# Kernel tuning notes

Measured on AMD Instinct MI355X. Metric: run time of the kernel, lower is better.

The kernel has to match this reference:

```python
import jax, jax.numpy as jnp
import numpy as np

B, S, NC, ND, V = 16, 512, 10000, 10000, 128


def _rn(k, shape, scale=0.05):
    return jax.random.normal(k, shape, dtype=jnp.float32) * scale


def setup_inputs() -> dict:
    key = jax.random.key(0)
    ks = jax.random.split(key, 24)
    inp = {
        'c_seq': jax.random.randint(ks[0], (B, S), 0, NC),
        'd_seq': jax.random.randint(ks[1], (B, S), 0, ND),
        'r_seq': jax.random.uniform(ks[2], (B, S), dtype=jnp.float32),
        # embeddings / vectors
        'D1_w': _rn(ks[3], (ND, 1)),
        'D2_w': _rn(ks[4], (ND, V)),
        'v_r': _rn(ks[5], (V,)),
        'v_beta': _rn(ks[6], (V,)),
        # GRU (torch layout: gates ordered r,z,n; W_ih [3V,2V], W_hh [3V,V])
        'W_ih': _rn(ks[7], (3 * V, 2 * V)),
        'W_hh': _rn(ks[8], (3 * V, V)),
        'b_ih': jnp.zeros((3 * V,), jnp.float32),
        'b_hh': jnp.zeros((3 * V,), jnp.float32),
        # linear_1: V -> V -> V -> 1 (weights stored [in, out])
        'm1_W1': _rn(ks[9], (V, V)), 'm1_b1': jnp.zeros((V,), jnp.float32),
        'm1_W2': _rn(ks[10], (V, V)), 'm1_b2': jnp.zeros((V,), jnp.float32),
        'm1_W3': _rn(ks[11], (V, 1)), 'm1_b3': jnp.zeros((1,), jnp.float32),
        # linear_2: 3V -> V -> V -> 1
        'm2_W1': _rn(ks[12], (3 * V, V)), 'm2_b1': jnp.zeros((V,), jnp.float32),
        'm2_W2': _rn(ks[13], (V, V)), 'm2_b2': jnp.zeros((V,), jnp.float32),
        'm2_W3': _rn(ks[14], (V, 1)), 'm2_b3': jnp.zeros((1,), jnp.float32),
    }
    return inp


def _mlp(x, W1, b1, W2, b2, W3, b3):
    h = jax.nn.relu(x @ W1 + b1)
    h = jax.nn.relu(h @ W2 + b2)
    return h @ W3 + b3


def _gru_seq(x, W_ih, W_hh, b_ih, b_hh):
    # x: [B,S,2V] -> h_seq [B,S,V]; torch GRU gate order r,z,n
    xp = x @ W_ih.T + b_ih  # [B,S,3V]

    def step(h, xt):
        hp = h @ W_hh.T + b_hh
        xr, xz, xn = jnp.split(xt, 3, axis=-1)
        hr, hz, hn = jnp.split(hp, 3, axis=-1)
        r = jax.nn.sigmoid(xr + hr)
        z = jax.nn.sigmoid(xz + hz)
        n = jnp.tanh(xn + r * hn)
        h_new = (1.0 - z) * n + z * h
        return h_new, h_new

    h0 = jnp.zeros((x.shape[0], W_hh.shape[1]), x.dtype)
    _, hs = jax.lax.scan(step, h0, jnp.swapaxes(xp, 0, 1))  # [S,B,V]
    return jnp.swapaxes(hs, 0, 1)


def reference(c_seq, d_seq, r_seq, D1_w, D2_w, v_r, v_beta,
              W_ih, W_hh, b_ih, b_hh,
              m1_W1, m1_b1, m1_W2, m1_b2, m1_W3, m1_b3,
              m2_W1, m2_b1, m2_W2, m2_b2, m2_W3, m2_b3):
    v_d_seq = D2_w[d_seq]                     # [B,S,V]
    v_r_seq = r_seq[..., None] * v_r          # [B,S,V]

    h_seq = _gru_seq(jnp.concatenate([v_d_seq, v_r_seq], axis=-1),
                     W_ih, W_hh, b_ih, b_hh)  # [B,S,V]
    alpha_seq = _mlp(h_seq, m1_W1, m1_b1, m1_W2, m1_b2, m1_W3, m1_b3)[..., 0]  # [B,S]

    bidx = jnp.arange(c_seq.shape[0])

    def step(C, ins):
        c_t, vd_t, vr_t = ins                 # [B], [B,V], [B,V]
        beta_prev = C[bidx, c_t]              # gather: [B]
        v_beta_prev = beta_prev[:, None] * v_beta  # [B,V]
        new_c = _mlp(jnp.concatenate([v_beta_prev, vd_t, vr_t], axis=-1),
                     m2_W1, m2_b1, m2_W2, m2_b2, m2_W3, m2_b3)[:, 0]  # [B]
        C = C.at[bidx, c_t].set(new_c)        # scatter
        return C, (C, new_c)

    C0 = jnp.zeros((c_seq.shape[0], NC), jnp.float32)
    _, (C_seq, beta_seq) = jax.lax.scan(
        step, C0,
        (jnp.swapaxes(c_seq, 0, 1), jnp.swapaxes(v_d_seq, 0, 1), jnp.swapaxes(v_r_seq, 0, 1)))
    C_seq = jnp.swapaxes(C_seq, 0, 1)[..., None]   # [B,S,NC,1]
    beta_seq = jnp.swapaxes(beta_seq, 0, 1)        # [B,S]

    gamma_seq = D1_w[d_seq][..., 0]                # [B,S]
    return (alpha_seq, beta_seq, gamma_seq, h_seq, C_seq)
```

## Files before the change

### kernel.cpp

```cpp
#include <hip/hip_runtime.h>

#define Bq   16
#define Sq   512
#define Vq   128
#define NCq  10000

typedef __attribute__((ext_vector_type(8))) short short8v;
typedef __attribute__((ext_vector_type(4))) float f32x4;

#define OFF_P1B_U  3145728u
#define OFF_WTIH   2097152u
#define OFF_WVRIH  2146304u
#define OFF_WVR1   2146688u
#define OFF_WVB    2146816u
#define OFF_PO     2146944u

#define PLN 136
#define PLSZ (16*PLN+8)

__device__ __forceinline__ unsigned short f2bf(float x) {
    unsigned u = __builtin_bit_cast(unsigned, x);
    unsigned r = (u + 0x7fffu + ((u >> 16) & 1u)) >> 16;
    return (unsigned short)r;
}
__device__ __forceinline__ float bfhi(unsigned u) {
    return __builtin_bit_cast(float, u << 16);
}
__device__ __forceinline__ float bflo(unsigned u) {
    return __builtin_bit_cast(float, u & 0xffff0000u);
}
__device__ __forceinline__ void gload_lds16(const void* g, void* l) {
    __builtin_amdgcn_global_load_lds(
        (const __attribute__((address_space(1))) unsigned int*)g,
        (__attribute__((address_space(3))) unsigned int*)l, 16, 0, 0);
}

__global__ __launch_bounds__(256) void k0_prep(
    const int* __restrict__ c_seq, const int* __restrict__ d_seq,
    const float* __restrict__ D1_w,
    const float* __restrict__ W_ih,
    const float* __restrict__ v_r, const float* __restrict__ v_beta,
    const float* __restrict__ m2W1,
    float* __restrict__ ws, float* __restrict__ gamma_out)
{
    const int blk = blockIdx.x, tid = threadIdx.x;

    if (blk < 128) {
        float* WTIH = ws + OFF_WTIH;
        int base = blk * 384;
        for (int i = tid; i < 384; i += 256) {
            int e = base + i;
            int k = e / 384, g = e % 384;
            WTIH[e] = W_ih[g * 256 + k];
        }
    } else if (blk == 128) {
        float* WVRIH = ws + OFF_WVRIH;
        float* WVR1  = ws + OFF_WVR1;
        float* WVB   = ws + OFF_WVB;
        for (int g = tid; g < 384; g += 256) {
            float a = 0.f;
            for (int k = 0; k < 128; ++k) a = fmaf(v_r[k], W_ih[g * 256 + 128 + k], a);
            WVRIH[g] = a;
        }
        if (tid < 128) {
            float a = 0.f, b = 0.f;
            for (int k = 0; k < 128; ++k) {
                a = fmaf(v_r[k],    m2W1[(256 + k) * 128 + tid], a);
                b = fmaf(v_beta[k], m2W1[k * 128 + tid],         b);
            }
            WVR1[tid] = a; WVB[tid] = b;
        }
    } else if (blk < 145) {
        const int b = blk - 129;
        __shared__ int cs[Sq];
        for (int i = tid; i < Sq; i += 256) cs[i] = c_seq[b * Sq + i];
        __syncthreads();
        int* PO = (int*)(ws + OFF_PO);
        for (int t = tid; t < Sq; t += 256) {
            int c = cs[t];
            int po = -1;
            for (int u = t - 1; u >= 0; --u) if (cs[u] == c) { po = u; break; }
            PO[t * 16 + b] = po;
        }
    } else {
        const int b = blk - 145;
        for (int s = tid; s < Sq; s += 256)
            gamma_out[b * Sq + s] = D1_w[d_seq[b * Sq + s]];
    }
}

__global__ __launch_bounds__(256) void k1_gemm(
    const int* __restrict__ d_seq, const float* __restrict__ D2_w,
    const float* __restrict__ m2W1,
    const float* __restrict__ b_ih, const float* __restrict__ b_hh,
    const float* __restrict__ r_seq, const float* __restrict__ m2b1,
    float* __restrict__ ws)
{
    __shared__ float As[64 * 128];
    __shared__ float Bs[128 * 64];
    const int blk = blockIdx.x, tid = threadIdx.x;
    const int nc = blk & 7;
    const int m0 = (blk >> 3) * 64;
    const float* WTIH = ws + OFF_WTIH;

    const float4* D2v = (const float4*)D2_w;
    for (int e = tid; e < 2048; e += 256) {
        int r = e >> 5, q = e & 31;
        int d = d_seq[m0 + r];
        *(float4*)&As[r * 128 + 4 * q] = D2v[d * 32 + q];
    }
    for (int e = tid; e < 2048; e += 256) {
        int k = e >> 4, q = e & 15;
        float4 v;
        if (nc < 6) v = *(const float4*)&WTIH[k * 384 + nc * 64 + 4 * q];
        else        v = *(const float4*)&m2W1[(128 + k) * 128 + (nc - 6) * 64 + 4 * q];
        *(float4*)&Bs[k * 64 + 4 * q] = v;
    }
    __syncthreads();

    const int tx = tid & 15, ty = tid >> 4;
    const int c0 = 4 * tx, r0 = 4 * ty;
    float acc[4][4];
#pragma unroll
    for (int i = 0; i < 4; ++i)
#pragma unroll
        for (int j = 0; j < 4; ++j) acc[i][j] = 0.f;

    for (int k = 0; k < 128; ++k) {
        float4 bv = *(const float4*)&Bs[k * 64 + c0];
#pragma unroll
        for (int i = 0; i < 4; ++i) {
            float a = As[(r0 + i) * 128 + k];
            acc[i][0] = fmaf(a, bv.x, acc[i][0]);
            acc[i][1] = fmaf(a, bv.y, acc[i][1]);
            acc[i][2] = fmaf(a, bv.z, acc[i][2]);
            acc[i][3] = fmaf(a, bv.w, acc[i][3]);
        }
    }

    float rsv[4];
#pragma unroll
    for (int i = 0; i < 4; ++i) rsv[i] = r_seq[m0 + r0 + i];

    if (nc < 6) {
        const int grow0 = nc * 64 + c0;
        float4 bi  = *(const float4*)&b_ih[grow0];
        float4 wv4 = *(const float4*)&(ws + OFF_WVRIH)[grow0];
        float4 bh4 = make_float4(0.f, 0.f, 0.f, 0.f);
        if (nc < 4) bh4 = *(const float4*)&b_hh[grow0];
        unsigned short* XPB = (unsigned short*)ws;
        const int r4 = grow0 >> 2;
#pragma unroll
        for (int i = 0; i < 4; ++i) {
            int row = m0 + r0 + i;
            int t = row & 511, bb = row >> 9;
            float vx = acc[i][0] + bi.x + bh4.x + rsv[i] * wv4.x;
            float vy = acc[i][1] + bi.y + bh4.y + rsv[i] * wv4.y;
            float vz = acc[i][2] + bi.z + bh4.z + rsv[i] * wv4.z;
            float vw = acc[i][3] + bi.w + bh4.w + rsv[i] * wv4.w;
            uint2 p;
            p.x = (unsigned)f2bf(vx) | ((unsigned)f2bf(vy) << 16);
            p.y = (unsigned)f2bf(vz) | ((unsigned)f2bf(vw) << 16);
            *(uint2*)&XPB[((size_t)((bb >> 2) * 512 + t)) * 1536 + r4 * 16 + (bb & 3) * 4] = p;
        }
    } else {
        const int j0 = (nc - 6) * 64 + c0;
        float4 b1v = *(const float4*)&m2b1[j0];
        float4 wr1 = *(const float4*)&(ws + OFF_WVR1)[j0];
        unsigned short* P1B = (unsigned short*)ws + OFF_P1B_U;
#pragma unroll
        for (int i = 0; i < 4; ++i) {
            int row = m0 + r0 + i;
            int t = row & 511, bb = row >> 9;
            float vx = acc[i][0] + b1v.x + rsv[i] * wr1.x;
            float vy = acc[i][1] + b1v.y + rsv[i] * wr1.y;
            float vz = acc[i][2] + b1v.z + rsv[i] * wr1.z;
            float vw = acc[i][3] + b1v.w + rsv[i] * wr1.w;
            uint2 p;
            p.x = (unsigned)f2bf(vx) | ((unsigned)f2bf(vy) << 16);
            p.y = (unsigned)f2bf(vz) | ((unsigned)f2bf(vw) << 16);
            *(uint2*)&P1B[((size_t)(t * 16 + bb)) * 128 + j0] = p;
        }
    }
}

__global__ __launch_bounds__(512, 1) void k2_scan(
    const float* __restrict__ W_hh, const float* __restrict__ b_hh,
    const float* __restrict__ m2W2, const float* __restrict__ m2b2,
    const float* __restrict__ m2W3, const float* __restrict__ m2b3,
    float* __restrict__ ws,
    float* __restrict__ hseq_out, float* __restrict__ beta_out)
{
    __shared__ __align__(16) unsigned char smem[23040];
    const int tid = threadIdx.x;
    const int l = tid & 63, wv = tid >> 6;
    const int qq = l >> 4, cb = l & 15;
    const int bgid = blockIdx.x;

    if (bgid < 4) {
        unsigned short* hP  = (unsigned short*)smem;
        unsigned short* xps = (unsigned short*)(smem + 4 * PLSZ);
        const unsigned short* XPB = (const unsigned short*)ws;

        short8v aH[3][4];
#pragma unroll
        for (int g = 0; g < 3; ++g) {
            const float* wrow = W_hh + (g * 128 + 16 * wv + cb) * 128;
#pragma unroll
            for (int kf = 0; kf < 4; ++kf) {
                short8v hi;
#pragma unroll
                for (int e = 0; e < 8; ++e) hi[e] = (short)f2bf(wrow[kf * 32 + qq * 8 + e]);
                aH[g][kf] = hi;
            }
        }
        float bhn[4];
        *(float4*)bhn = *(const float4*)&b_hh[256 + 16 * wv + 4 * qq];
        float hold[4] = {0.f, 0.f, 0.f, 0.f};

        for (int i = tid; i < 2 * PLSZ; i += 512) hP[i] = 0;
        if (wv < 3) {
            const unsigned short* src = XPB + ((size_t)(bgid * 512)) * 1536 + wv * 512 + l * 8;
            gload_lds16(src, xps + wv * 512);
        }
        __syncthreads();

        for (int t = 0; t < 512; ++t) {
            if (t < 511 && wv < 3) {
                const unsigned short* src =
                    XPB + ((size_t)(bgid * 512 + t + 1)) * 1536 + wv * 512 + l * 8;
                gload_lds16(src, xps + ((t + 1) & 1) * 1536 + wv * 512);
            }
            const unsigned short* xcur = xps + (t & 1) * 1536;
            f32x4 px[3];
#pragma unroll
            for (int g = 0; g < 3; ++g) {
                uint2 u = *(const uint2*)(xcur + (32 * g + 4 * wv + qq) * 16 + (cb & 3) * 4);
                px[g][0] = bfhi(u.x); px[g][1] = bflo(u.x);
                px[g][2] = bfhi(u.y); px[g][3] = bflo(u.y);
            }
            const unsigned short* HI = hP + (t & 1) * PLSZ;
            unsigned short* HIn = hP + ((t + 1) & 1) * PLSZ;

            f32x4 C0 = {0.f,0.f,0.f,0.f}, C1 = {0.f,0.f,0.f,0.f}, C2 = {0.f,0.f,0.f,0.f};
#pragma unroll
            for (int kf = 0; kf < 4; ++kf) {
                short8v Bh = *(const short8v*)(HI + cb * PLN + kf * 32 + qq * 8);
                C0 = __builtin_amdgcn_mfma_f32_16x16x32_bf16(aH[0][kf], Bh, C0, 0, 0, 0);
                C1 = __builtin_amdgcn_mfma_f32_16x16x32_bf16(aH[1][kf], Bh, C1, 0, 0, 0);
                C2 = __builtin_amdgcn_mfma_f32_16x16x32_bf16(aH[2][kf], Bh, C2, 0, 0, 0);
            }
            float hnew[4];
#pragma unroll
            for (int i = 0; i < 4; ++i) {
                float pr = C0[i] + px[0][i];
                float pz = C1[i] + px[1][i];
                float r = 1.f / (1.f + __expf(-pr));
                float z = 1.f / (1.f + __expf(-pz));
                float hn = C2[i] + bhn[i];
                float npre = fmaf(r, hn, px[2][i]);
                float ax = fabsf(npre);
                float e2 = __expf(-2.f * ax);
                float n = copysignf((1.f - e2) / (1.f + e2), npre);
                float hv = (1.f - z) * n + z * hold[i];
                hold[i] = hv;
                hnew[i] = hv;
            }
            if (cb < 4) {
                *(float4*)&hseq_out[((size_t)((bgid * 4 + cb) * 512 + t)) * 128 + 16 * wv + 4 * qq] =
                    make_float4(hnew[0], hnew[1], hnew[2], hnew[3]);
                unsigned short h0 = f2bf(hnew[0]), h1 = f2bf(hnew[1]);
                unsigned short h2 = f2bf(hnew[2]), h3 = f2bf(hnew[3]);
                uint2 hw;
                hw.x = (unsigned)h0 | ((unsigned)h1 << 16);
                hw.y = (unsigned)h2 | ((unsigned)h3 << 16);
                *(uint2*)(HIn + cb * PLN + 16 * wv + 4 * qq) = hw;
            }
            __syncthreads();
        }
    } else {
        const int bq = bgid - 4;
        float* bhL = (float*)smem;
        int*   poT = (int*)(smem + 8192);
        unsigned short* h1P  = (unsigned short*)(smem + 16384);
        unsigned short* xpre = (unsigned short*)(smem + 20752);
        float* redL = (float*)(smem + 22800);
        const unsigned short* P1B = (const unsigned short*)ws + OFF_P1B_U;

        {
            const int* POg = (const int*)(ws + OFF_PO);
            for (int i = tid; i < 2048; i += 512)
                poT[i] = POg[(i >> 2) * 16 + 4 * bq + (i & 3)];
        }
        for (int i = tid; i < PLSZ; i += 512) h1P[i] = 0;
        if (wv == 0)
            gload_lds16(P1B + ((size_t)(4 * bq)) * 128 + l * 8, xpre);

        short8v aH[4];
#pragma unroll
        for (int kf = 0; kf < 4; ++kf) {
            short8v hi;
#pragma unroll
            for (int e = 0; e < 8; ++e)
                hi[e] = (short)f2bf(m2W2[(kf * 32 + qq * 8 + e) * 128 + 16 * wv + cb]);
            aH[kf] = hi;
        }
        float w3C[4], b2C[4];
        *(float4*)w3C = *(const float4*)&m2W3[16 * wv + 4 * qq];
        *(float4*)b2C = *(const float4*)&m2b2[16 * wv + 4 * qq];
        const float b3v = m2b3[0];

        const int bb2 = tid & 3, j4 = (tid >> 2) & 31;
        const bool pa = tid < 128;
        float wvb[4] = {0.f, 0.f, 0.f, 0.f};
        if (pa) *(float4*)wvb = *(const float4*)&(ws + OFF_WVB)[j4 * 4];
        float btap = 0.f;
        __syncthreads();

        for (int t = 0; t < 512; ++t) {
            if (pa) {
                int po = poT[t * 4 + bb2];
                float bp = (po == t - 1) ? btap : ((po >= 0) ? bhL[bb2 * 512 + po] : 0.f);
                uint2 u = *(const uint2*)(xpre + (t & 1) * 512 + bb2 * 128 + j4 * 4);
                float h0 = fmaxf(0.f, fmaf(bp, wvb[0], bfhi(u.x)));
                float h1 = fmaxf(0.f, fmaf(bp, wvb[1], bflo(u.x)));
                float h2 = fmaxf(0.f, fmaf(bp, wvb[2], bfhi(u.y)));
                float h3 = fmaxf(0.f, fmaf(bp, wvb[3], bflo(u.y)));
                uint2 hw;
                hw.x = (unsigned)f2bf(h0) | ((unsigned)f2bf(h1) << 16);
                hw.y = (unsigned)f2bf(h2) | ((unsigned)f2bf(h3) << 16);
                *(uint2*)(h1P + bb2 * PLN + j4 * 4) = hw;
            }
            if (tid < 4 && t > 0) bhL[tid * 512 + (t - 1)] = btap;
            __syncthreads();

            if (t < 511 && wv == 0)
                gload_lds16(P1B + ((size_t)((t + 1) * 16 + 4 * bq)) * 128 + l * 8,
                            xpre + ((t + 1) & 1) * 512);

            f32x4 C = {0.f, 0.f, 0.f, 0.f};
#pragma unroll
            for (int kf = 0; kf < 4; ++kf) {
                short8v Bh = *(const short8v*)(h1P + cb * PLN + kf * 32 + qq * 8);
                C = __builtin_amdgcn_mfma_f32_16x16x32_bf16(aH[kf], Bh, C, 0, 0, 0);
            }
            float part = 0.f;
#pragma unroll
            for (int i = 0; i < 4; ++i)
                part = fmaf(fmaxf(0.f, C[i] + b2C[i]), w3C[i], part);
            part += __shfl_xor(part, 16);
            part += __shfl_xor(part, 32);
            if (qq == 0 && cb < 4) redL[wv * 4 + cb] = part;
            __syncthreads();

            float bta = b3v;
#pragma unroll
            for (int w = 0; w < 8; ++w) bta += redL[w * 4 + (tid & 3)];
            btap = bta;
        }
        if (tid < 4) bhL[tid * 512 + 511] = btap;
        __syncthreads();
        for (int i = tid; i < 2048; i += 512)
            beta_out[(4 * bq + (i >> 9)) * 512 + (i & 511)] = bhL[i];
    }
}

__global__ __launch_bounds__(256) void k2b_fill(
    const int* __restrict__ c_seq, const float* __restrict__ beta_in,
    float* __restrict__ C_out)
{
    __shared__ int   scs[Sq];
    __shared__ float sbt[Sq];
    const int bid = blockIdx.x, tid = threadIdx.x;
    const int b = bid / 40, rem = bid % 40;
    const int chunk = rem >> 2, q = rem & 3;

    for (int i = tid; i < Sq; i += 256) {
        scs[i] = c_seq[b * Sq + i];
        sbt[i] = beta_in[b * Sq + i];
    }
    __syncthreads();

    const int c0 = chunk * 1024 + tid * 4;
    if (c0 >= NCq) return;

    float cur0 = 0.f, cur1 = 0.f, cur2 = 0.f, cur3 = 0.f;
    const int tlo = q * 128, thi = tlo + 128;
    float* base = C_out + (size_t)b * Sq * NCq + c0;

    for (int t = 0; t < tlo; ++t) {
        int ct = scs[t] - c0; float bv = sbt[t];
        cur0 = (ct == 0) ? bv : cur0;
        cur1 = (ct == 1) ? bv : cur1;
        cur2 = (ct == 2) ? bv : cur2;
        cur3 = (ct == 3) ? bv : cur3;
    }
    for (int t = tlo; t < thi; ++t) {
        int ct = scs[t] - c0; float bv = sbt[t];
        cur0 = (ct == 0) ? bv : cur0;
        cur1 = (ct == 1) ? bv : cur1;
        cur2 = (ct == 2) ? bv : cur2;
        cur3 = (ct == 3) ? bv : cur3;
        *(float4*)(base + (size_t)t * NCq) = make_float4(cur0, cur1, cur2, cur3);
    }
}

__global__ __launch_bounds__(256) void k3_alpha(
    const float* __restrict__ hseq,
    const float* __restrict__ W1, const float* __restrict__ b1,
    const float* __restrict__ W2, const float* __restrict__ b2,
    const float* __restrict__ W3, const float* __restrict__ b3,
    float* __restrict__ alpha_out)
{
    __shared__ float Hs[32 * 128];
    __shared__ float T1[32 * 128];
    __shared__ float red[4][16];
    const int blk = blockIdx.x, tid = threadIdx.x;
    const int row0 = blk * 32;

    for (int e = tid; e < 1024; e += 256) {
        int r = e >> 5, q = e & 31;
        *(float4*)&Hs[r * 128 + 4 * q] =
            *(const float4*)&hseq[(size_t)(row0 + r) * 128 + 4 * q];
    }
    __syncthreads();

    const int j = tid & 127, rh = tid >> 7;
    const float b1j = b1[j], b2j = b2[j], w3j = W3[j];
    float acc[16];
#pragma unroll
    for (int r = 0; r < 16; ++r) acc[r] = b1j;
    for (int k = 0; k < 128; ++k) {
        float w = W1[k * 128 + j];
#pragma unroll
        for (int r = 0; r < 16; ++r)
            acc[r] = fmaf(Hs[(rh * 16 + r) * 128 + k], w, acc[r]);
    }
#pragma unroll
    for (int r = 0; r < 16; ++r) {
        acc[r] = fmaxf(acc[r], 0.f);
        T1[(rh * 16 + r) * 128 + j] = acc[r];
    }
    __syncthreads();
    float acc2[16];
#pragma unroll
    for (int r = 0; r < 16; ++r) acc2[r] = b2j;
    for (int k = 0; k < 128; ++k) {
        float w = W2[k * 128 + j];
#pragma unroll
        for (int r = 0; r < 16; ++r)
            acc2[r] = fmaf(T1[(rh * 16 + r) * 128 + k], w, acc2[r]);
    }
#pragma unroll
    for (int r = 0; r < 16; ++r) {
        float p = fmaxf(acc2[r], 0.f) * w3j;
#pragma unroll
        for (int off = 1; off < 64; off <<= 1) p += __shfl_xor(p, off);
        if ((tid & 63) == 0) red[tid >> 6][r] = p;
    }
    __syncthreads();
    if (tid < 32) {
        int rr = tid & 15, g = tid >> 4;
        alpha_out[row0 + g * 16 + rr] = red[2 * g][rr] + red[2 * g + 1][rr] + b3[0];
    }
}

extern "C" void kernel_launch(void* const* d_in, const int* in_sizes, int n_in,
                              void* d_out, int out_size, void* d_ws, size_t ws_size,
                              hipStream_t stream) {
    const int*   c_seq = (const int*)d_in[0];
    const int*   d_seq = (const int*)d_in[1];
    const float* r_seq = (const float*)d_in[2];
    const float* D1_w  = (const float*)d_in[3];
    const float* D2_w  = (const float*)d_in[4];
    const float* v_r   = (const float*)d_in[5];
    const float* v_b   = (const float*)d_in[6];
    const float* W_ih  = (const float*)d_in[7];
    const float* W_hh  = (const float*)d_in[8];
    const float* b_ih  = (const float*)d_in[9];
    const float* b_hh  = (const float*)d_in[10];
    const float* m1W1  = (const float*)d_in[11];
    const float* m1b1  = (const float*)d_in[12];
    const float* m1W2  = (const float*)d_in[13];
    const float* m1b2  = (const float*)d_in[14];
    const float* m1W3  = (const float*)d_in[15];
    const float* m1b3  = (const float*)d_in[16];
    const float* m2W1  = (const float*)d_in[17];
    const float* m2b1  = (const float*)d_in[18];
    const float* m2W2  = (const float*)d_in[19];
    const float* m2b2  = (const float*)d_in[20];
    const float* m2W3  = (const float*)d_in[21];
    const float* m2b3  = (const float*)d_in[22];

    float* out   = (float*)d_out;
    float* alpha = out;
    float* beta  = out + 8192;
    float* gamma = out + 16384;
    float* hseq  = out + 24576;
    float* Cseq  = out + 1073152;
    float* ws    = (float*)d_ws;

    hipLaunchKernelGGL(k0_prep, dim3(161), dim3(256), 0, stream,
                       c_seq, d_seq, D1_w, W_ih, v_r, v_b, m2W1, ws, gamma);
    hipLaunchKernelGGL(k1_gemm, dim3(1024), dim3(256), 0, stream,
                       d_seq, D2_w, m2W1, b_ih, b_hh, r_seq, m2b1, ws);
    hipLaunchKernelGGL(k2_scan, dim3(8), dim3(512), 0, stream,
                       W_hh, b_hh, m2W2, m2b2, m2W3, m2b3, ws, hseq, beta);
    hipLaunchKernelGGL(k2b_fill, dim3(640), dim3(256), 0, stream,
                       c_seq, beta, Cseq);
    hipLaunchKernelGGL(k3_alpha, dim3(256), dim3(256), 0, stream,
                       hseq, m1W1, m1b1, m1W2, m1b2, m1W3, m1b3, alpha);
}
```

Measured before the change: 750.7 us.

## Register-prefetch scan inputs and use lightweight LDS-only barriers in recurrent scans

Both recurrent scan loops stop staging per-step inputs through LDS via global_load_lds and instead prefetch them two steps ahead into registers. __syncthreads is replaced by a barrier that only waits on LDS counters, so global loads and stores in flight no longer stall each step. The beta scan also drops the poT LDS table, loading previous-occurrence indices directly with lookahead, and uses a transposed reduction buffer read with float4. The gate math switches to hardware reciprocal approximations, which slightly changes precision. The lgkm-only barrier depends on the outstanding global loads being register-destined, not LDS-destined.

```diff
diff --git a/kernel.cpp b/kernel.cpp
--- a/kernel.cpp
+++ b/kernel.cpp
@@ -29,10 +29,11 @@
 __device__ __forceinline__ float bflo(unsigned u) {
     return __builtin_bit_cast(float, u & 0xffff0000u);
 }
-__device__ __forceinline__ void gload_lds16(const void* g, void* l) {
-    __builtin_amdgcn_global_load_lds(
-        (const __attribute__((address_space(1))) unsigned int*)g,
-        (__attribute__((address_space(3))) unsigned int*)l, 16, 0, 0);
+__device__ __forceinline__ void barrier_lgkm() {
+    asm volatile("s_waitcnt lgkmcnt(0)" ::: "memory");
+    __builtin_amdgcn_sched_barrier(0);
+    __builtin_amdgcn_s_barrier();
+    __builtin_amdgcn_sched_barrier(0);
 }
 
 __global__ __launch_bounds__(256) void k0_prep(
@@ -191,53 +192,58 @@
     float* __restrict__ ws,
     float* __restrict__ hseq_out, float* __restrict__ beta_out)
 {
-    __shared__ __align__(16) unsigned char smem[23040];
+    __shared__ __align__(16) unsigned char smem[12800];
     const int tid = threadIdx.x;
     const int l = tid & 63, wv = tid >> 6;
     const int qq = l >> 4, cb = l & 15;
     const int bgid = blockIdx.x;
 
     if (bgid < 4) {
-        unsigned short* hP  = (unsigned short*)smem;
-        unsigned short* xps = (unsigned short*)(smem + 4 * PLSZ);
+        unsigned short* hP = (unsigned short*)smem;
         const unsigned short* XPB = (const unsigned short*)ws;
 
-        short8v aH[3][4];
-#pragma unroll
-        for (int g = 0; g < 3; ++g) {
-            const float* wrow = W_hh + (g * 128 + 16 * wv + cb) * 128;
-#pragma unroll
-            for (int kf = 0; kf < 4; ++kf) {
-                short8v hi;
-#pragma unroll
-                for (int e = 0; e < 8; ++e) hi[e] = (short)f2bf(wrow[kf * 32 + qq * 8 + e]);
-                aH[g][kf] = hi;
-            }
+        short8v aH0[4], aH1[4], aH2[4];
+#pragma unroll
+        for (int kf = 0; kf < 4; ++kf) {
+            const int kb = kf * 32 + qq * 8;
+            const float* w0 = W_hh + (0 * 128 + 16 * wv + cb) * 128 + kb;
+            const float* w1 = W_hh + (1 * 128 + 16 * wv + cb) * 128 + kb;
+            const float* w2 = W_hh + (2 * 128 + 16 * wv + cb) * 128 + kb;
+            short8v h0, h1, h2;
+#pragma unroll
+            for (int e = 0; e < 8; ++e) {
+                h0[e] = (short)f2bf(w0[e]);
+                h1[e] = (short)f2bf(w1[e]);
+                h2[e] = (short)f2bf(w2[e]);
+            }
+            aH0[kf] = h0; aH1[kf] = h1; aH2[kf] = h2;
         }
         float bhn[4];
         *(float4*)bhn = *(const float4*)&b_hh[256 + 16 * wv + 4 * qq];
+
+        const size_t pbase = (size_t)(bgid * 512) * 1536 + (4 * wv + qq) * 16 + (cb & 3) * 4;
+        uint2 pxA0 = *(const uint2*)(XPB + pbase);
+        uint2 pxA1 = *(const uint2*)(XPB + pbase + 512);
+        uint2 pxA2 = *(const uint2*)(XPB + pbase + 1024);
+        uint2 pxB0 = *(const uint2*)(XPB + pbase + 1536);
+        uint2 pxB1 = *(const uint2*)(XPB + pbase + 1536 + 512);
+        uint2 pxB2 = *(const uint2*)(XPB + pbase + 1536 + 1024);
+
+        float* hp = hseq_out + ((size_t)((bgid * 4 + (cb & 3)) * 512)) * 128 + 16 * wv + 4 * qq;
         float hold[4] = {0.f, 0.f, 0.f, 0.f};
-
         for (int i = tid; i < 2 * PLSZ; i += 512) hP[i] = 0;
-        if (wv < 3) {
-            const unsigned short* src = XPB + ((size_t)(bgid * 512)) * 1536 + wv * 512 + l * 8;
-            gload_lds16(src, xps + wv * 512);
-        }
         __syncthreads();
 
         for (int t = 0; t < 512; ++t) {
-            if (t < 511 && wv < 3) {
-                const unsigned short* src =
-                    XPB + ((size_t)(bgid * 512 + t + 1)) * 1536 + wv * 512 + l * 8;
-                gload_lds16(src, xps + ((t + 1) & 1) * 1536 + wv * 512);
-            }
-            const unsigned short* xcur = xps + (t & 1) * 1536;
-            f32x4 px[3];
-#pragma unroll
-            for (int g = 0; g < 3; ++g) {
-                uint2 u = *(const uint2*)(xcur + (32 * g + 4 * wv + qq) * 16 + (cb & 3) * 4);
-                px[g][0] = bfhi(u.x); px[g][1] = bflo(u.x);
-                px[g][2] = bfhi(u.y); px[g][3] = bflo(u.y);
+            float pf0[4] = {bfhi(pxA0.x), bflo(pxA0.x), bfhi(pxA0.y), bflo(pxA0.y)};
+            float pf1[4] = {bfhi(pxA1.x), bflo(pxA1.x), bfhi(pxA1.y), bflo(pxA1.y)};
+            float pf2[4] = {bfhi(pxA2.x), bflo(pxA2.x), bfhi(pxA2.y), bflo(pxA2.y)};
+            pxA0 = pxB0; pxA1 = pxB1; pxA2 = pxB2;
+            if (t < 510) {
+                const unsigned short* s = XPB + pbase + (size_t)(t + 2) * 1536;
+                pxB0 = *(const uint2*)(s);
+                pxB1 = *(const uint2*)(s + 512);
+                pxB2 = *(const uint2*)(s + 1024);
             }
             const unsigned short* HI = hP + (t & 1) * PLSZ;
             unsigned short* HIn = hP + ((t + 1) & 1) * PLSZ;
@@ -246,55 +252,42 @@
 #pragma unroll
             for (int kf = 0; kf < 4; ++kf) {
                 short8v Bh = *(const short8v*)(HI + cb * PLN + kf * 32 + qq * 8);
-                C0 = __builtin_amdgcn_mfma_f32_16x16x32_bf16(aH[0][kf], Bh, C0, 0, 0, 0);
-                C1 = __builtin_amdgcn_mfma_f32_16x16x32_bf16(aH[1][kf], Bh, C1, 0, 0, 0);
-                C2 = __builtin_amdgcn_mfma_f32_16x16x32_bf16(aH[2][kf], Bh, C2, 0, 0, 0);
+                C0 = __builtin_amdgcn_mfma_f32_16x16x32_bf16(aH0[kf], Bh, C0, 0, 0, 0);
+                C1 = __builtin_amdgcn_mfma_f32_16x16x32_bf16(aH1[kf], Bh, C1, 0, 0, 0);
+                C2 = __builtin_amdgcn_mfma_f32_16x16x32_bf16(aH2[kf], Bh, C2, 0, 0, 0);
             }
             float hnew[4];
 #pragma unroll
             for (int i = 0; i < 4; ++i) {
-                float pr = C0[i] + px[0][i];
-                float pz = C1[i] + px[1][i];
-                float r = 1.f / (1.f + __expf(-pr));
-                float z = 1.f / (1.f + __expf(-pz));
+                float pr = C0[i] + pf0[i];
+                float pz = C1[i] + pf1[i];
+                float r = __builtin_amdgcn_rcpf(1.f + __expf(-pr));
+                float z = __builtin_amdgcn_rcpf(1.f + __expf(-pz));
                 float hn = C2[i] + bhn[i];
-                float npre = fmaf(r, hn, px[2][i]);
-                float ax = fabsf(npre);
-                float e2 = __expf(-2.f * ax);
-                float n = copysignf((1.f - e2) / (1.f + e2), npre);
-                float hv = (1.f - z) * n + z * hold[i];
+                float npre = fmaf(r, hn, pf2[i]);
+                float e2 = __expf(-2.f * fabsf(npre));
+                float n = copysignf((1.f - e2) * __builtin_amdgcn_rcpf(1.f + e2), npre);
+                float hv = fmaf(z, hold[i] - n, n);
                 hold[i] = hv;
                 hnew[i] = hv;
             }
             if (cb < 4) {
-                *(float4*)&hseq_out[((size_t)((bgid * 4 + cb) * 512 + t)) * 128 + 16 * wv + 4 * qq] =
-                    make_float4(hnew[0], hnew[1], hnew[2], hnew[3]);
-                unsigned short h0 = f2bf(hnew[0]), h1 = f2bf(hnew[1]);
-                unsigned short h2 = f2bf(hnew[2]), h3 = f2bf(hnew[3]);
+                *(float4*)hp = make_float4(hnew[0], hnew[1], hnew[2], hnew[3]);
                 uint2 hw;
-                hw.x = (unsigned)h0 | ((unsigned)h1 << 16);
-                hw.y = (unsigned)h2 | ((unsigned)h3 << 16);
+                hw.x = (unsigned)f2bf(hnew[0]) | ((unsigned)f2bf(hnew[1]) << 16);
+                hw.y = (unsigned)f2bf(hnew[2]) | ((unsigned)f2bf(hnew[3]) << 16);
                 *(uint2*)(HIn + cb * PLN + 16 * wv + 4 * qq) = hw;
             }
-            __syncthreads();
+            hp += 128;
+            barrier_lgkm();
         }
     } else {
         const int bq = bgid - 4;
         float* bhL = (float*)smem;
-        int*   poT = (int*)(smem + 8192);
-        unsigned short* h1P  = (unsigned short*)(smem + 16384);
-        unsigned short* xpre = (unsigned short*)(smem + 20752);
-        float* redL = (float*)(smem + 22800);
+        unsigned short* h1P = (unsigned short*)(smem + 8192);
+        float* redT = (float*)(smem + 8192 + 2 * PLSZ);
         const unsigned short* P1B = (const unsigned short*)ws + OFF_P1B_U;
-
-        {
-            const int* POg = (const int*)(ws + OFF_PO);
-            for (int i = tid; i < 2048; i += 512)
-                poT[i] = POg[(i >> 2) * 16 + 4 * bq + (i & 3)];
-        }
-        for (int i = tid; i < PLSZ; i += 512) h1P[i] = 0;
-        if (wv == 0)
-            gload_lds16(P1B + ((size_t)(4 * bq)) * 128 + l * 8, xpre);
+        const int* POg = (const int*)(ws + OFF_PO);
 
         short8v aH[4];
 #pragma unroll
@@ -310,34 +303,47 @@
         *(float4*)b2C = *(const float4*)&m2b2[16 * wv + 4 * qq];
         const float b3v = m2b3[0];
 
+        const bool pa = (tid < 128);
         const int bb2 = tid & 3, j4 = (tid >> 2) & 31;
-        const bool pa = tid < 128;
         float wvb[4] = {0.f, 0.f, 0.f, 0.f};
-        if (pa) *(float4*)wvb = *(const float4*)&(ws + OFF_WVB)[j4 * 4];
-        float btap = 0.f;
+        uint2 p1A = {0, 0}, p1B = {0, 0};
+        int poCur = -1, poNxt = -1;
+        float bpPre = 0.f, btap = 0.f;
+        if (pa) {
+            *(float4*)wvb = *(const float4*)&(ws + OFF_WVB)[j4 * 4];
+            p1A = *(const uint2*)(P1B + (size_t)(0 * 16 + 4 * bq + bb2) * 128 + j4 * 4);
+            p1B = *(const uint2*)(P1B + (size_t)(1 * 16 + 4 * bq + bb2) * 128 + j4 * 4);
+            poCur = POg[0 * 16 + 4 * bq + bb2];
+            poNxt = POg[1 * 16 + 4 * bq + bb2];
+        }
+        for (int i = tid; i < PLSZ; i += 512) h1P[i] = 0;
         __syncthreads();
 
         for (int t = 0; t < 512; ++t) {
             if (pa) {
-                int po = poT[t * 4 + bb2];
-                float bp = (po == t - 1) ? btap : ((po >= 0) ? bhL[bb2 * 512 + po] : 0.f);
-                uint2 u = *(const uint2*)(xpre + (t & 1) * 512 + bb2 * 128 + j4 * 4);
-                float h0 = fmaxf(0.f, fmaf(bp, wvb[0], bfhi(u.x)));
-                float h1 = fmaxf(0.f, fmaf(bp, wvb[1], bflo(u.x)));
-                float h2 = fmaxf(0.f, fmaf(bp, wvb[2], bfhi(u.y)));
-                float h3 = fmaxf(0.f, fmaf(bp, wvb[3], bflo(u.y)));
+                float bp = (poCur == t - 1) ? btap : bpPre;
+                float f0 = bfhi(p1A.x), f1 = bflo(p1A.x);
+                float f2v = bfhi(p1A.y), f3 = bflo(p1A.y);
+                float h0 = fmaxf(0.f, fmaf(bp, wvb[0], f0));
+                float h1 = fmaxf(0.f, fmaf(bp, wvb[1], f1));
+                float h2 = fmaxf(0.f, fmaf(bp, wvb[2], f2v));
+                float h3 = fmaxf(0.f, fmaf(bp, wvb[3], f3));
                 uint2 hw;
                 hw.x = (unsigned)f2bf(h0) | ((unsigned)f2bf(h1) << 16);
                 hw.y = (unsigned)f2bf(h2) | ((unsigned)f2bf(h3) << 16);
                 *(uint2*)(h1P + bb2 * PLN + j4 * 4) = hw;
-            }
-            if (tid < 4 && t > 0) bhL[tid * 512 + (t - 1)] = btap;
-            __syncthreads();
-
-            if (t < 511 && wv == 0)
-                gload_lds16(P1B + ((size_t)((t + 1) * 16 + 4 * bq)) * 128 + l * 8,
-                            xpre + ((t + 1) & 1) * 512);
-
+                p1A = p1B;
+                if (t < 510)
+                    p1B = *(const uint2*)(P1B + (size_t)((t + 2) * 16 + 4 * bq + bb2) * 128 + j4 * 4);
+            }
+            barrier_lgkm();
+
+            if (pa) {
+                bpPre = 0.f;
+                if (poNxt >= 0 && poNxt < t) bpPre = bhL[bb2 * 512 + poNxt];
+                poCur = poNxt;
+                if (t < 510) poNxt = POg[(t + 2) * 16 + 4 * bq + bb2];
+            }
             f32x4 C = {0.f, 0.f, 0.f, 0.f};
 #pragma unroll
             for (int kf = 0; kf < 4; ++kf) {
@@ -350,15 +356,18 @@
                 part = fmaf(fmaxf(0.f, C[i] + b2C[i]), w3C[i], part);
             part += __shfl_xor(part, 16);
             part += __shfl_xor(part, 32);
-            if (qq == 0 && cb < 4) redL[wv * 4 + cb] = part;
-            __syncthreads();
-
-            float bta = b3v;
-#pragma unroll
-            for (int w = 0; w < 8; ++w) bta += redL[w * 4 + (tid & 3)];
-            btap = bta;
-        }
-        if (tid < 4) bhL[tid * 512 + 511] = btap;
+            if (qq == 0 && cb < 4) redT[cb * 8 + wv] = part;
+            barrier_lgkm();
+
+            if (pa) {
+                float4 ra = *(const float4*)&redT[bb2 * 8];
+                float4 rb = *(const float4*)&redT[bb2 * 8 + 4];
+                float bta = ((ra.x + ra.y) + (ra.z + ra.w)) +
+                            ((rb.x + rb.y) + (rb.z + rb.w)) + b3v;
+                if (j4 == 0) bhL[bb2 * 512 + t] = bta;
+                btap = bta;
+            }
+        }
         __syncthreads();
         for (int i = tid; i < 2048; i += 512)
             beta_out[(4 * bq + (i >> 9)) * 512 + (i & 511)] = bhL[i];
```

Measured after the change: 636.6 us. 1.18x faster.
